# Kernel optimization log

Measured on AMD Instinct MI355X. Metric: run time of the kernel, lower is better.

The kernel has to match this reference:

```python
import jax, jax.numpy as jnp
import numpy as np
from jax import lax

LRELU_SLOPE = 0.2
EPS = 1e-8


def eq_linear(x, W, b):
    # EqualizedLinear: weight scaled by 1/sqrt(fan_in)
    c = 1.0 / np.sqrt(W.shape[1])
    return x @ (W * c).T + b


def mod_conv(x, s, W, demod):
    # x: [b, cin, h, w], s: [b, cin], W: [cout, cin, k, k]
    b, cin, h, w = x.shape
    cout, _, k, _ = W.shape
    c = 1.0 / np.sqrt(cin * k * k)
    weights = (W * c)[None] * s[:, None, :, None, None]  # [b, cout, cin, k, k]
    if demod:
        sigma_inv = lax.rsqrt(jnp.sum(weights ** 2, axis=(2, 3, 4)) + EPS)  # [b, cout]
        weights = weights * sigma_inv[:, :, None, None, None]
    x2 = x.reshape(1, b * cin, h, w)
    wk = weights.reshape(b * cout, cin, k, k)
    pad = k // 2
    out = lax.conv_general_dilated(
        x2, wk, window_strides=(1, 1), padding=[(pad, pad), (pad, pad)],
        dimension_numbers=("NCHW", "OIHW", "NCHW"), feature_group_count=b)
    return out.reshape(b, cout, h, w)


def style_block(x, w, noise, style_W, style_b, conv_W, scale_noise, bias):
    A = eq_linear(w, style_W, style_b)          # [b, cin]
    x = mod_conv(x, A, conv_W, demod=True)      # [b, cout, h, w]
    if noise is not None:
        x = x + scale_noise[None, :, None, None] * noise
    return jax.nn.leaky_relu(x + bias[None, :, None, None], LRELU_SLOPE)


def rgb_block(x, w, style_W, style_b, conv_W, bias):
    A = eq_linear(w, style_W, style_b)
    x = mod_conv(x, A, conv_W, demod=False)     # 1x1 conv to 3 channels
    return jax.nn.leaky_relu(x + bias[None, :, None, None], LRELU_SLOPE)


def setup_inputs() -> dict:
    key = jax.random.key(0)
    ks = jax.random.split(key, 10)
    B, CIN, COUT, WD, H, W = 8, 512, 512, 512, 64, 64
    return {
        "x": jax.random.normal(ks[0], (B, CIN, H, W), jnp.float32),
        "w": jax.random.normal(ks[1], (B, WD), jnp.float32),
        "noise": jax.random.normal(ks[2], (2, B, 1, H, W), jnp.float32),
        # StyleBlock 1
        "s1_style_W": jax.random.normal(ks[3], (CIN, WD), jnp.float32),
        "s1_style_b": jnp.ones((CIN,), jnp.float32),
        "s1_conv_W": jax.random.normal(ks[4], (COUT, CIN, 3, 3), jnp.float32),
        "s1_scale_noise": jnp.zeros((1,), jnp.float32),
        "s1_bias": jnp.zeros((COUT,), jnp.float32),
        # StyleBlock 2
        "s2_style_W": jax.random.normal(ks[5], (COUT, WD), jnp.float32),
        "s2_style_b": jnp.ones((COUT,), jnp.float32),
        "s2_conv_W": jax.random.normal(ks[6], (COUT, COUT, 3, 3), jnp.float32),
        "s2_scale_noise": jnp.zeros((1,), jnp.float32),
        "s2_bias": jnp.zeros((COUT,), jnp.float32),
        # RGBBlock
        "rgb_style_W": jax.random.normal(ks[7], (COUT, WD), jnp.float32),
        "rgb_style_b": jnp.ones((COUT,), jnp.float32),
        "rgb_conv_W": jax.random.normal(ks[8], (3, COUT, 1, 1), jnp.float32),
        "rgb_bias": jnp.zeros((3,), jnp.float32),
    }


def reference(x, w, noise,
              s1_style_W, s1_style_b, s1_conv_W, s1_scale_noise, s1_bias,
              s2_style_W, s2_style_b, s2_conv_W, s2_scale_noise, s2_bias,
              rgb_style_W, rgb_style_b, rgb_conv_W, rgb_bias):
    x = style_block(x, w, noise[0], s1_style_W, s1_style_b, s1_conv_W, s1_scale_noise, s1_bias)
    x = style_block(x, w, noise[1], s2_style_W, s2_style_b, s2_conv_W, s2_scale_noise, s2_bias)
    rgb = rgb_block(x, w, rgb_style_W, rgb_style_b, rgb_conv_W, rgb_bias)
    return (x, rgb)
```

## Files before the change

kernel.cpp:

```cpp
#include <hip/hip_runtime.h>
#include <stdint.h>

typedef __attribute__((ext_vector_type(8))) short bf16x8;
typedef __attribute__((ext_vector_type(4))) float f32x4;

__device__ __forceinline__ ushort f2bf(float f) {
  uint32_t u = __builtin_bit_cast(uint32_t, f);
  u += 0x7fffu + ((u >> 16) & 1u);
  return (ushort)(u >> 16);
}

__device__ __forceinline__ void async_copy16(const void* gsrc, void* ldst) {
  __builtin_amdgcn_global_load_lds(
      (const __attribute__((address_space(1))) void*)gsrc,
      (__attribute__((address_space(3))) void*)ldst, 16, 0, 0);
}

__global__ void style_linear(const float* __restrict__ w, const float* __restrict__ sW,
                             const float* __restrict__ sb, float* __restrict__ A) {
  const int b = blockIdx.x;
  const int co = blockIdx.y * 128 + threadIdx.x;
  const float c = 0.04419417382415922f;
  const float* wr = w + b * 512;
  const float* Wr = sW + (size_t)co * 512;
  float s = 0.f;
  for (int d = 0; d < 512; ++d) s += wr[d] * Wr[d];
  A[b * 512 + co] = s * c + sb[co];
}

__global__ void prep_sigma(const float* __restrict__ Wc, const float* __restrict__ A,
                           ushort* __restrict__ Wt, float* __restrict__ sig) {
  const int co = blockIdx.x;
  const int ci = threadIdx.x;
  const int lane = ci & 63, wid = ci >> 6;
  const float c = 0.014731391274719738f;
  const float* src = Wc + ((size_t)co * 512 + ci) * 9;
  float s = 0.f;
#pragma unroll
  for (int t = 0; t < 9; ++t) {
    float v = src[t] * c;
    Wt[(size_t)t * 262144 + co * 512 + ci] = f2bf(v);
    s += v * v;
  }
  __shared__ float red[8][8];
#pragma unroll
  for (int b = 0; b < 8; ++b) {
    float a = A[b * 512 + ci];
    float v = s * a * a;
#pragma unroll
    for (int off = 32; off; off >>= 1) v += __shfl_xor(v, off);
    if (lane == 0) red[b][wid] = v;
  }
  __syncthreads();
  if (ci < 8) {
    float t = 0.f;
#pragma unroll
    for (int wv = 0; wv < 8; ++wv) t += red[ci][wv];
    sig[ci * 512 + co] = rsqrtf(t + 1e-8f);
  }
}

__global__ void zero_border(uint4* __restrict__ x1, uint4* __restrict__ x2) {
  const int i = blockIdx.x * 256 + threadIdx.x;
  const int per = 16640;
  const int tot = per * 8;
  if (i >= 2 * tot) return;
  uint4* base = (i < tot) ? x1 : x2;
  int t = (i < tot) ? i : i - tot;
  const int bb = t / per;
  int r = t - bb * per;
  int row, cell, q;
  if (r < 8448) {
    row = (r >= 4224) ? 65 : 0;
    int pos = (r >= 4224) ? r - 4224 : r;
    cell = pos >> 6;
    q = pos & 63;
  } else {
    int r2 = r - 8448;
    row = 1 + (r2 >> 7);
    cell = ((r2 >> 6) & 1) ? 65 : 0;
    q = r2 & 63;
  }
  base[(((size_t)bb * 66 + row) * 66 + cell) * 64 + q] = make_uint4(0u, 0u, 0u, 0u);
}

__global__ void mod_transpose(const float* __restrict__ X, const float* __restrict__ A,
                              ushort* __restrict__ xs) {
  __shared__ float tile[128][65];
  const int h = blockIdx.x;
  const int ci0 = blockIdx.y * 128;
  const int b = blockIdx.z;
  const int tid = threadIdx.x;
  const int wcol = tid & 63;
  const int r0 = tid >> 6;
#pragma unroll 4
  for (int i = 0; i < 32; ++i) {
    const int cil = r0 + i * 4;
    const int ci = ci0 + cil;
    const size_t off = ((size_t)(b * 512 + ci) * 64 + h) * 64 + wcol;
    tile[cil][wcol] = X[off] * A[b * 512 + ci];
  }
  __syncthreads();
  const int sub = tid & 3;
  const int w = tid >> 2;
  ushort* dst = xs + (((size_t)b * 66 + (h + 1)) * 66 + (w + 1)) * 512 + ci0 + sub * 32;
#pragma unroll
  for (int g = 0; g < 4; ++g) {
    bf16x8 v;
#pragma unroll
    for (int j = 0; j < 8; ++j) v[j] = (short)f2bf(tile[sub * 32 + g * 8 + j][w]);
    *(bf16x8*)(dst + g * 8) = v;
  }
}

#define WAITVM(N) asm volatile("s_waitcnt vmcnt(" #N ")" ::: "memory")

#define PHASE(S, WN, DOSTAGE)                                                        \
  do {                                                                               \
    WAITVM(WN);                                                                      \
    asm volatile("" ::: "memory");                                                   \
    __builtin_amdgcn_s_barrier();                                                    \
    asm volatile("" ::: "memory");                                                   \
    const int q_ = (S) & 3;                                                          \
    const char* baA = (const char*)(&smA[0][0] + q_ * 8192);                         \
    const char* baB = (const char*)(&smB[0][0] + q_ * 8192);                         \
    bf16x8 af[8], bv[4];                                                             \
    _Pragma("unroll") for (int m_ = 0; m_ < 8; ++m_)                                 \
        af[m_] = *(const bf16x8*)(baA + aro[m_]);                                    \
    _Pragma("unroll") for (int n_ = 0; n_ < 4; ++n_)                                 \
        bv[n_] = *(const bf16x8*)(baB + bro[n_]);                                    \
    if (DOSTAGE) stage((S) + 3);                                                     \
    asm volatile("s_waitcnt lgkmcnt(0)" ::: "memory");                               \
    __builtin_amdgcn_sched_barrier(0);                                               \
    __builtin_amdgcn_s_setprio(1);                                                   \
    _Pragma("unroll") for (int m_ = 0; m_ < 8; ++m_)                                 \
      _Pragma("unroll") for (int n_ = 0; n_ < 4; ++n_)                               \
        acc[m_][n_] = __builtin_amdgcn_mfma_f32_16x16x32_bf16(af[m_], bv[n_],        \
                                                              acc[m_][n_], 0, 0, 0); \
    __builtin_amdgcn_s_setprio(0);                                                   \
    __builtin_amdgcn_sched_barrier(0);                                               \
  } while (0)

template <int OUT_MODE>
__global__ __launch_bounds__(512, 2) void conv3x3(
    const ushort* __restrict__ xs, const ushort* __restrict__ Wt,
    const float* __restrict__ sig, const float* __restrict__ noise,
    const float* __restrict__ scale_noise, const float* __restrict__ bias,
    const float* __restrict__ amod, void* __restrict__ outp) {
  __shared__ __align__(16) ushort smA[4][8192];
  __shared__ __align__(16) ushort smB[4][8192];
  const int tid = threadIdx.x, lane = tid & 63, wid = tid >> 6;
  const int wr = wid >> 2, wc = wid & 3;
  const int b = blockIdx.z;
  const int co0 = blockIdx.x * 256;
  const int px0 = blockIdx.y * 256;
  const int h0 = px0 >> 6;

  const int sswz = ((lane & 3) ^ ((lane >> 3) & 3)) * 8;
  int aoff[2], boff[2];
  ushort *ldsA[2], *ldsB[2];
#pragma unroll
  for (int i = 0; i < 2; ++i) {
    const int row = (i * 8 + wid) * 16 + (lane >> 2);
    aoff[i] = (co0 + row) * 512 + sswz;
    const int hh = h0 + (row >> 6), ww = row & 63;
    boff[i] = ((b * 66 + hh) * 66 + ww) * 512 + sswz;
    ldsA[i] = &smA[0][0] + (i * 8 + wid) * 512 + lane * 8;
    ldsB[i] = &smB[0][0] + (i * 8 + wid) * 512 + lane * 8;
  }
  const int rdsw = ((lane >> 4) ^ ((lane >> 1) & 3)) * 16;
  int aro[8], bro[4];
#pragma unroll
  for (int m = 0; m < 8; ++m) aro[m] = (wr * 128 + m * 16 + (lane & 15)) * 64 + rdsw;
#pragma unroll
  for (int n = 0; n < 4; ++n) bro[n] = (wc * 64 + n * 16 + (lane & 15)) * 64 + rdsw;

  f32x4 acc[8][4];
#pragma unroll
  for (int m = 0; m < 8; ++m)
#pragma unroll
    for (int n = 0; n < 4; ++n) acc[m][n] = (f32x4){0.f, 0.f, 0.f, 0.f};

  auto stage = [&](int s) {
    const int tap = s >> 4;
    const int ci0 = (s & 15) << 5;
    const int kh = tap / 3;
    const int kw = tap - kh * 3;
    const int q = s & 3;
    const ushort* Wb = Wt + tap * 262144 + ci0;
    const ushort* Xb = xs + (kh * 66 + kw) * 512 + ci0;
    async_copy16(Wb + aoff[0], ldsA[0] + q * 8192);
    async_copy16(Wb + aoff[1], ldsA[1] + q * 8192);
    async_copy16(Xb + boff[0], ldsB[0] + q * 8192);
    async_copy16(Xb + boff[1], ldsB[1] + q * 8192);
  };

  stage(0);
  stage(1);
  stage(2);

  for (int s = 0; s < 140; s += 4) {
    PHASE(s + 0, 8, true);
    PHASE(s + 1, 8, true);
    PHASE(s + 2, 8, true);
    PHASE(s + 3, 8, true);
  }
  PHASE(140, 8, true);
  PHASE(141, 8, false);
  PHASE(142, 4, false);
  PHASE(143, 0, false);

  const float sn = scale_noise[0];
  const int colp = lane & 15;
  const int rq = (lane >> 4) * 4;
  float nz[4];
#pragma unroll
  for (int n = 0; n < 4; ++n)
    nz[n] = sn * noise[b * 4096 + px0 + wc * 64 + n * 16 + colp];
#pragma unroll
  for (int m = 0; m < 8; ++m) {
    const int cob = co0 + wr * 128 + m * 16 + rq;
    float sg[4], bs[4], am[4];
#pragma unroll
    for (int r = 0; r < 4; ++r) {
      sg[r] = sig[b * 512 + cob + r];
      bs[r] = bias[cob + r];
      am[r] = (OUT_MODE == 0) ? amod[b * 512 + cob + r] : 0.f;
    }
#pragma unroll
    for (int n = 0; n < 4; ++n) {
      const int px = px0 + wc * 64 + n * 16 + colp;
      if (OUT_MODE == 0) {
        const int hh = px >> 6, ww = px & 63;
        ushort pk[4];
#pragma unroll
        for (int r = 0; r < 4; ++r) {
          float v = acc[m][n][r] * sg[r] + nz[n] + bs[r];
          v = (v > 0.f) ? v : 0.2f * v;
          pk[r] = f2bf(v * am[r]);
        }
        uint2 u;
        u.x = (uint32_t)pk[0] | ((uint32_t)pk[1] << 16);
        u.y = (uint32_t)pk[2] | ((uint32_t)pk[3] << 16);
        *(uint2*)((ushort*)outp + (((size_t)b * 66 + hh + 1) * 66 + (ww + 1)) * 512 + cob) = u;
      } else {
#pragma unroll
        for (int r = 0; r < 4; ++r) {
          float v = acc[m][n][r] * sg[r] + nz[n] + bs[r];
          v = (v > 0.f) ? v : 0.2f * v;
          ((float*)outp)[((size_t)b * 512 + cob + r) * 4096 + px] = v;
        }
      }
    }
  }
}

__global__ void rgb_k(const float* __restrict__ X, const float* __restrict__ Ar,
                      const float* __restrict__ rgbW, const float* __restrict__ rgbB,
                      float* __restrict__ out) {
  __shared__ float wmod[3 * 512];
  const int b = blockIdx.y;
  const int tid = threadIdx.x;
  const float c = 0.04419417382415922f;
  for (int idx = tid; idx < 1536; idx += 256)
    wmod[idx] = rgbW[idx] * c * Ar[b * 512 + (idx & 511)];
  __syncthreads();
  const int p = blockIdx.x * 256 + tid;
  const float* xb = X + (size_t)b * 512 * 4096 + p;
  float a0 = 0.f, a1 = 0.f, a2 = 0.f;
  for (int ci = 0; ci < 512; ++ci) {
    float xv = xb[(size_t)ci * 4096];
    a0 += wmod[ci] * xv;
    a1 += wmod[512 + ci] * xv;
    a2 += wmod[1024 + ci] * xv;
  }
  float v0 = a0 + rgbB[0], v1 = a1 + rgbB[1], v2 = a2 + rgbB[2];
  v0 = (v0 > 0.f) ? v0 : 0.2f * v0;
  v1 = (v1 > 0.f) ? v1 : 0.2f * v1;
  v2 = (v2 > 0.f) ? v2 : 0.2f * v2;
  out[((size_t)b * 3 + 0) * 4096 + p] = v0;
  out[((size_t)b * 3 + 1) * 4096 + p] = v1;
  out[((size_t)b * 3 + 2) * 4096 + p] = v2;
}

extern "C" void kernel_launch(void* const* d_in, const int* in_sizes, int n_in,
                              void* d_out, int out_size, void* d_ws, size_t ws_size,
                              hipStream_t stream) {
  const float* x     = (const float*)d_in[0];
  const float* w     = (const float*)d_in[1];
  const float* noise = (const float*)d_in[2];
  const float* s1_sW = (const float*)d_in[3];
  const float* s1_sb = (const float*)d_in[4];
  const float* s1_cW = (const float*)d_in[5];
  const float* s1_sn = (const float*)d_in[6];
  const float* s1_b  = (const float*)d_in[7];
  const float* s2_sW = (const float*)d_in[8];
  const float* s2_sb = (const float*)d_in[9];
  const float* s2_cW = (const float*)d_in[10];
  const float* s2_sn = (const float*)d_in[11];
  const float* s2_b  = (const float*)d_in[12];
  const float* r_sW  = (const float*)d_in[13];
  const float* r_sb  = (const float*)d_in[14];
  const float* r_cW  = (const float*)d_in[15];
  const float* r_b   = (const float*)d_in[16];

  char* ws = (char*)d_ws;
  float*  A1  = (float*)(ws + 0);
  float*  A2  = (float*)(ws + 16384);
  float*  Arr = (float*)(ws + 32768);
  float*  sg1 = (float*)(ws + 49152);
  float*  sg2 = (float*)(ws + 65536);
  ushort* Wt1 = (ushort*)(ws + 98304);
  ushort* xs1 = (ushort*)(ws + 4816896);
  ushort* Wt2 = (ushort*)(ws + 4816896);
  ushort* xs2 = (ushort*)(ws + 40501248);
  float* outx   = (float*)d_out;
  float* outrgb = outx + (size_t)8 * 512 * 4096;

  style_linear<<<dim3(8, 4), 128, 0, stream>>>(w, s1_sW, s1_sb, A1);
  style_linear<<<dim3(8, 4), 128, 0, stream>>>(w, s2_sW, s2_sb, A2);
  style_linear<<<dim3(8, 4), 128, 0, stream>>>(w, r_sW, r_sb, Arr);

  prep_sigma<<<512, 512, 0, stream>>>(s1_cW, A1, Wt1, sg1);

  zero_border<<<1040, 256, 0, stream>>>((uint4*)xs1, (uint4*)xs2);
  mod_transpose<<<dim3(64, 4, 8), 256, 0, stream>>>(x, A1, xs1);

  conv3x3<0><<<dim3(2, 16, 8), 512, 0, stream>>>(xs1, Wt1, sg1, noise, s1_sn, s1_b, A2,
                                                 (void*)xs2);
  prep_sigma<<<512, 512, 0, stream>>>(s2_cW, A2, Wt2, sg2);
  conv3x3<1><<<dim3(2, 16, 8), 512, 0, stream>>>(xs2, Wt2, sg2, noise + 32768, s2_sn, s2_b,
                                                 sg2, (void*)outx);
  rgb_k<<<dim3(16, 8), 256, 0, stream>>>(outx, Arr, r_cW, r_b, outrgb);
}
```

Before: 381.5 us.

## Parallelize style linear per wave, flatten conv grid, drop explicit lgkm wait

The style linear kernel now gives each output channel its own wave, which reads the weight row with coalesced lanes and combines the partial sums with a shuffle reduction. The old version had each thread loop serially over 512 strided elements. The conv grid is flattened to 1D with batch in the low bits, so concurrently scheduled blocks share the same weight tiles. The explicit lgkmcnt(0) wait before the MFMA block is removed, which leaves the compiler to insert waits for the LDS reads. That is a correctness risk if the compiler does not insert them across the sched_barrier.

```diff
diff --git a/kernel.cpp b/kernel.cpp
--- a/kernel.cpp
+++ b/kernel.cpp
@@ -18,14 +18,21 @@
 
 __global__ void style_linear(const float* __restrict__ w, const float* __restrict__ sW,
                              const float* __restrict__ sb, float* __restrict__ A) {
-  const int b = blockIdx.x;
-  const int co = blockIdx.y * 128 + threadIdx.x;
+  const int b = blockIdx.y;
+  const int lane = threadIdx.x & 63, wv = threadIdx.x >> 6;
+  const int co = blockIdx.x * 4 + wv;
   const float c = 0.04419417382415922f;
   const float* wr = w + b * 512;
   const float* Wr = sW + (size_t)co * 512;
   float s = 0.f;
-  for (int d = 0; d < 512; ++d) s += wr[d] * Wr[d];
-  A[b * 512 + co] = s * c + sb[co];
+#pragma unroll
+  for (int i = 0; i < 8; ++i) {
+    const int d = i * 64 + lane;
+    s += wr[d] * Wr[d];
+  }
+#pragma unroll
+  for (int off = 32; off; off >>= 1) s += __shfl_xor(s, off);
+  if (lane == 0) A[b * 512 + co] = s * c + sb[co];
 }
 
 __global__ void prep_sigma(const float* __restrict__ Wc, const float* __restrict__ A,
@@ -130,7 +137,6 @@
     _Pragma("unroll") for (int n_ = 0; n_ < 4; ++n_)                                 \
         bv[n_] = *(const bf16x8*)(baB + bro[n_]);                                    \
     if (DOSTAGE) stage((S) + 3);                                                     \
-    asm volatile("s_waitcnt lgkmcnt(0)" ::: "memory");                               \
     __builtin_amdgcn_sched_barrier(0);                                               \
     __builtin_amdgcn_s_setprio(1);                                                   \
     _Pragma("unroll") for (int m_ = 0; m_ < 8; ++m_)                                 \
@@ -151,9 +157,11 @@
   __shared__ __align__(16) ushort smB[4][8192];
   const int tid = threadIdx.x, lane = tid & 63, wid = tid >> 6;
   const int wr = wid >> 2, wc = wid & 3;
-  const int b = blockIdx.z;
-  const int co0 = blockIdx.x * 256;
-  const int px0 = blockIdx.y * 256;
+  const int id = blockIdx.x;
+  const int b = id & 7;
+  const int tile = id >> 3;
+  const int co0 = (tile & 1) * 256;
+  const int px0 = (tile >> 1) * 256;
   const int h0 = px0 >> 6;
 
   const int sswz = ((lane & 3) ^ ((lane >> 3) & 3)) * 8;
@@ -317,19 +325,18 @@
   float* outx   = (float*)d_out;
   float* outrgb = outx + (size_t)8 * 512 * 4096;
 
-  style_linear<<<dim3(8, 4), 128, 0, stream>>>(w, s1_sW, s1_sb, A1);
-  style_linear<<<dim3(8, 4), 128, 0, stream>>>(w, s2_sW, s2_sb, A2);
-  style_linear<<<dim3(8, 4), 128, 0, stream>>>(w, r_sW, r_sb, Arr);
+  style_linear<<<dim3(128, 8), 256, 0, stream>>>(w, s1_sW, s1_sb, A1);
+  style_linear<<<dim3(128, 8), 256, 0, stream>>>(w, s2_sW, s2_sb, A2);
+  style_linear<<<dim3(128, 8), 256, 0, stream>>>(w, r_sW, r_sb, Arr);
 
   prep_sigma<<<512, 512, 0, stream>>>(s1_cW, A1, Wt1, sg1);
 
   zero_border<<<1040, 256, 0, stream>>>((uint4*)xs1, (uint4*)xs2);
   mod_transpose<<<dim3(64, 4, 8), 256, 0, stream>>>(x, A1, xs1);
 
-  conv3x3<0><<<dim3(2, 16, 8), 512, 0, stream>>>(xs1, Wt1, sg1, noise, s1_sn, s1_b, A2,
-                                                 (void*)xs2);
+  conv3x3<0><<<dim3(256), 512, 0, stream>>>(xs1, Wt1, sg1, noise, s1_sn, s1_b, A2, (void*)xs2);
   prep_sigma<<<512, 512, 0, stream>>>(s2_cW, A2, Wt2, sg2);
-  conv3x3<1><<<dim3(2, 16, 8), 512, 0, stream>>>(xs2, Wt2, sg2, noise + 32768, s2_sn, s2_b,
-                                                 sg2, (void*)outx);
+  conv3x3<1><<<dim3(256), 512, 0, stream>>>(xs2, Wt2, sg2, noise + 32768, s2_sn, s2_b, sg2,
+                                            (void*)outx);
   rgb_k<<<dim3(16, 8), 256, 0, stream>>>(outx, Arr, r_cW, r_b, outrgb);
 }
```

After: 351.1 us. 8.0% less time.
